# Kernel tuning notes

Measured on AMD Instinct MI355X. Metric: run time of the kernel, lower is better.

The kernel has to match this reference:

```python
import jax, jax.numpy as jnp
import numpy as np

N = 50000        # nodes
E = 500000       # undirected edges (stored once)
D = 64           # n_in_features
DOUT = 64        # n_out_features
HLF = 2          # hl_factor
NCONV = 3        # n_conv_its
H = D * HLF      # hidden width of conv MLPs


def setup_inputs() -> dict:
    key = jax.random.key(0)
    ks = jax.random.split(key, 8)
    s = 0.05
    edge_features = jax.random.normal(ks[0], (E, D), jnp.float32)
    edge_index = jax.random.randint(ks[1], (2, E), 0, N, dtype=jnp.int64)
    node_w1 = jax.random.normal(ks[2], (NCONV, 2 * D, H), jnp.float32) * s
    node_b1 = jnp.zeros((NCONV, H), jnp.float32)
    node_w2 = jax.random.normal(ks[3], (NCONV, H, D), jnp.float32) * s
    node_b2 = jnp.zeros((NCONV, D), jnp.float32)
    edge_w1 = jax.random.normal(ks[4], (2 * D, H), jnp.float32) * s
    edge_b1 = jnp.zeros((H,), jnp.float32)
    edge_w2 = jax.random.normal(ks[5], (H, DOUT), jnp.float32) * s
    edge_b2 = jnp.zeros((DOUT,), jnp.float32)
    return dict(edge_features=edge_features, edge_index=edge_index,
                node_w1=node_w1, node_b1=node_b1, node_w2=node_w2, node_b2=node_b2,
                edge_w1=edge_w1, edge_b1=edge_b1, edge_w2=edge_w2, edge_b2=edge_b2)


def _seg_mean(x, idx, n):
    s = jax.ops.segment_sum(x, idx, num_segments=n)
    c = jax.ops.segment_sum(jnp.ones((idx.shape[0], 1), x.dtype), idx, num_segments=n)
    return s / jnp.maximum(c, 1.0)


def reference(edge_features, edge_index, node_w1, node_b1, node_w2, node_b2,
              edge_w1, edge_b1, edge_w2, edge_b2):
    src, dst = edge_index[0], edge_index[1]
    # bidirectional (symmetrized) edges for message passing
    bi_src = jnp.concatenate([src, dst])
    bi_dst = jnp.concatenate([dst, src])

    # EdgeConvNoNodes: node feature = mean of incident edge features
    x = _seg_mean(jnp.concatenate([edge_features, edge_features], axis=0), bi_dst, N)  # [N, D]

    # NodeConv layers with residual: message = MLP(cat[x_i, x_j]), mean-aggregated
    for i in range(NCONV):
        m = jnp.concatenate([x[bi_dst], x[bi_src]], axis=-1)        # [2E, 2D]
        m = jax.nn.relu(m @ node_w1[i] + node_b1[i])                # [2E, H]
        m = jax.nn.relu(m @ node_w2[i] + node_b2[i])                # [2E, D]
        x = x + _seg_mean(m, bi_dst, N)

    # EdgeConv: symmetric edge MLP over node endpoint pairs + symmetry side loss
    def emlp(a, b):
        h = jax.nn.relu(jnp.concatenate([a, b], axis=-1) @ edge_w1 + edge_b1)
        return h @ edge_w2 + edge_b2

    e1 = emlp(x[src], x[dst])   # [E, DOUT]
    e2 = emlp(x[dst], x[src])   # [E, DOUT]
    edge_out = 0.5 * (e1 + e2)
    side_loss = jnp.mean((e1 - e2) ** 2)
    return edge_out, side_loss
```

## Files before the change

kernel.cpp:

```cpp
#include <hip/hip_runtime.h>


#define NN 50000
#define NE 500000
#define DE 1000000
#define NEB 7813

typedef __attribute__((ext_vector_type(8))) __bf16 bfrag;
typedef __attribute__((ext_vector_type(8))) short  svec8;
typedef __attribute__((ext_vector_type(4))) float  f32x4;

__device__ __forceinline__ unsigned short f2bf(float f){
  unsigned u = __builtin_bit_cast(unsigned, f);
  u += 0x7fffu + ((u >> 16) & 1u);
  return (unsigned short)(u >> 16);
}
__device__ __forceinline__ float bf2f(unsigned short s){
  return __builtin_bit_cast(float, ((unsigned)s) << 16);
}
#define MFMA __builtin_amdgcn_mfma_f32_16x16x32_bf16

__device__ __forceinline__ bfrag hbuild(const unsigned short* __restrict__ p,
                                        const unsigned short* __restrict__ q){
  svec8 pv = *(const svec8*)p;
  svec8 qv = *(const svec8*)q;
  bfrag r;
  #pragma unroll
  for (int i = 0; i < 8; i++){
    float f = bf2f((unsigned short)pv[i]) + bf2f((unsigned short)qv[i]);
    f = f > 0.f ? f : 0.f;
    r[i] = (__bf16)f;
  }
  return r;
}

__global__ void k_hist(const int* __restrict__ ei, int* __restrict__ cnt){
  int e = blockIdx.x*256 + threadIdx.x;
  if (e >= DE) return;
  int dst = (e < NE) ? ei[NE + e] : ei[e - NE];
  atomicAdd(&cnt[dst], 1);
}

__global__ void k_scan(const int* __restrict__ cnt, int* __restrict__ off,
                       int* __restrict__ cur, float* __restrict__ dinv){
  __shared__ int wsum[16];
  const int CH = 49;
  int tid = threadIdx.x;
  int base = tid * CH;
  int s = 0;
  for (int i = 0; i < CH; i++){
    int idx = base + i;
    if (idx < NN) s += cnt[idx];
  }
  int lane = tid & 63, w = tid >> 6;
  int inc = s;
  for (int o2 = 1; o2 < 64; o2 <<= 1){
    int t = __shfl_up(inc, o2);
    if (lane >= o2) inc += t;
  }
  if (lane == 63) wsum[w] = inc;
  __syncthreads();
  if (tid < 16){
    int v = wsum[tid], p = v;
    for (int o2 = 1; o2 < 16; o2 <<= 1){
      int t = __shfl_up(p, o2, 16);
      if (tid >= o2) p += t;
    }
    wsum[tid] = p - v;
  }
  __syncthreads();
  int pre = wsum[w] + inc - s;
  for (int i = 0; i < CH; i++){
    int idx = base + i;
    if (idx < NN){
      int v = cnt[idx];
      off[idx] = pre; cur[idx] = pre;
      dinv[idx] = 1.0f / (float)(v > 1 ? v : 1);
      pre += v;
    }
  }
  if (tid == 0) off[NN] = DE;
}

__global__ void k_fill(const int* __restrict__ ei, int* __restrict__ cur,
                       int* __restrict__ nbr, int* __restrict__ dstA, int* __restrict__ eid){
  int e = blockIdx.x*256 + threadIdx.x;
  if (e >= DE) return;
  int s, d, id;
  if (e < NE){ s = ei[e];  d = ei[NE + e]; id = e;      }
  else       { s = ei[e];  d = ei[e - NE]; id = e - NE; }
  int pos = atomicAdd(&cur[d], 1);
  nbr[pos] = s; dstA[pos] = d; eid[pos] = id;
}

__global__ void k_pack(const float* __restrict__ nw1, const float* __restrict__ nw2,
                       const float* __restrict__ ew1, const float* __restrict__ ew2,
                       unsigned short* __restrict__ wp){
  int t = blockIdx.x*256 + threadIdx.x;
  if (t >= 98304) return;
  const float* src; int NO, p, base;
  if (t < 49152)      { int l = t/16384;            src = nw1 + l*16384; NO=128; p = t - l*16384;      base = t - p; }
  else if (t < 73728) { int q = t-49152; int l=q/8192; src = nw2 + l*8192; NO=64; p = q - l*8192;      base = t - p; }
  else if (t < 90112) {                              src = ew1;           NO=128; p = t - 73728;       base = 73728; }
  else                {                              src = ew2;           NO=64;  p = t - 90112;       base = 90112; }
  int f = p >> 9, r = p & 511, lane = r >> 3, i = r & 7;
  int NB = NO >> 4, kb = f / NB, nb = f - kb*NB;
  int k = kb*32 + ((lane >> 4) << 3) + i;
  int c = nb*16 + (lane & 15);
  wp[base + p] = f2bf(src[k*NO + c]);
}

__global__ void k_init(const float* __restrict__ ef, const int* __restrict__ off,
                       const int* __restrict__ eid, const float* __restrict__ dinv,
                       float* __restrict__ x, unsigned short* __restrict__ xbf){
  int n = blockIdx.x*4 + (threadIdx.x >> 6);
  int lane = threadIdx.x & 63;
  if (n >= NN) return;
  int s0 = off[n], s1 = off[n+1];
  float acc = 0.f;
  for (int s = s0; s < s1; s++) acc += ef[eid[s]*64 + lane];
  float v = acc * dinv[n];
  x[n*64 + lane] = v;
  xbf[n*64 + lane] = f2bf(v);
}

__global__ __launch_bounds__(256,2) void k_pq(
    const unsigned short* __restrict__ xbf,
    const unsigned short* __restrict__ wp, int w1off,
    const float* __restrict__ bias,
    unsigned short* __restrict__ pb, unsigned short* __restrict__ qb)
{
  int lane = threadIdx.x & 63, wid = threadIdx.x >> 6;
  int tile = (blockIdx.x*4 + wid) * 32;
  if (tile >= NN) return;
  int r16 = lane & 15, g = lane >> 4;
  const svec8* w1g = (const svec8*)(wp + w1off);
  bfrag a[2][2];
  #pragma unroll
  for (int rb = 0; rb < 2; rb++){
    int n = tile + rb*16 + r16; if (n >= NN) n = NN-1;
    #pragma unroll
    for (int kb = 0; kb < 2; kb++)
      a[rb][kb] = __builtin_bit_cast(bfrag, *(const svec8*)(xbf + n*64 + kb*32 + g*8));
  }
  for (int ph = 0; ph < 2; ph++){
    f32x4 acc[8][2];
    #pragma unroll
    for (int nb = 0; nb < 8; nb++){ acc[nb][0] = (f32x4){0,0,0,0}; acc[nb][1] = (f32x4){0,0,0,0}; }
    #pragma unroll
    for (int kb = 0; kb < 2; kb++){
      #pragma unroll
      for (int nb = 0; nb < 8; nb++){
        bfrag b = __builtin_bit_cast(bfrag, w1g[((ph*2+kb)*8+nb)*64 + lane]);
        acc[nb][0] = MFMA(a[0][kb], b, acc[nb][0], 0, 0, 0);
        acc[nb][1] = MFMA(a[1][kb], b, acc[nb][1], 0, 0, 0);
      }
    }
    unsigned short* ob = ph ? qb : pb;
    #pragma unroll
    for (int nb = 0; nb < 8; nb++){
      float bv = (ph == 0) ? bias[nb*16 + r16] : 0.f;
      #pragma unroll
      for (int rb = 0; rb < 2; rb++){
        #pragma unroll
        for (int j = 0; j < 4; j++){
          int n = tile + rb*16 + g*4 + j;
          if (n < NN) ob[n*128 + nb*16 + r16] = f2bf(acc[nb][rb][j] + bv);
        }
      }
    }
  }
}

__global__ __launch_bounds__(256,4) void k_conv(
    const unsigned short* __restrict__ pb, const unsigned short* __restrict__ qb,
    const int* __restrict__ cdst, const int* __restrict__ cnbr,
    const unsigned short* __restrict__ wp, int w2off,
    const float* __restrict__ b2, float* __restrict__ xsum)
{
  int lane = threadIdx.x & 63, wid = threadIdx.x >> 6;
  int tile = (blockIdx.x*4 + wid) * 32;
  if (tile >= DE) return;
  int r16 = lane & 15, g = lane >> 4;
  int dr = cdst[tile + (lane & 31)];
  int d0 = cdst[tile + r16],      d1 = cdst[tile + 16 + r16];
  int s0 = cnbr[tile + r16],      s1 = cnbr[tile + 16 + r16];
  const svec8* w2g = (const svec8*)(wp + w2off);

  f32x4 acc[4][2];
  #pragma unroll
  for (int nb = 0; nb < 4; nb++){ acc[nb][0] = (f32x4){0,0,0,0}; acc[nb][1] = (f32x4){0,0,0,0}; }

  #pragma unroll
  for (int kb = 0; kb < 4; kb++){
    int off = kb*32 + g*8;
    bfrag h0 = hbuild(pb + d0*128 + off, qb + s0*128 + off);
    bfrag h1 = hbuild(pb + d1*128 + off, qb + s1*128 + off);
    #pragma unroll
    for (int nb = 0; nb < 4; nb++){
      bfrag b = __builtin_bit_cast(bfrag, w2g[(kb*4+nb)*64 + lane]);
      acc[nb][0] = MFMA(h0, b, acc[nb][0], 0, 0, 0);
      acc[nb][1] = MFMA(h1, b, acc[nb][1], 0, 0, 0);
    }
  }
  float m[4][2][4];
  #pragma unroll
  for (int nb = 0; nb < 4; nb++){
    float bv = b2[nb*16 + r16];
    #pragma unroll
    for (int rb = 0; rb < 2; rb++){
      #pragma unroll
      for (int j = 0; j < 4; j++){
        float v = acc[nb][rb][j] + bv;
        m[nb][rb][j] = v > 0.f ? v : 0.f;
      }
    }
  }
  int prev = __shfl_up(dr, 1);
  bool flag = (lane < 32) && (lane == 0 || dr != prev);
  unsigned long long mask = __ballot(flag);
  while (mask){
    int s = (int)__builtin_ctzll(mask);
    mask &= mask - 1;
    int e = mask ? (int)__builtin_ctzll(mask) : 32;
    int dseg = __shfl(dr, s);
    float p0 = 0.f, p1 = 0.f, p2 = 0.f, p3 = 0.f;
    #pragma unroll
    for (int rb = 0; rb < 2; rb++){
      #pragma unroll
      for (int j = 0; j < 4; j++){
        int row = rb*16 + g*4 + j;
        if ((unsigned)(row - s) < (unsigned)(e - s)){
          p0 += m[0][rb][j]; p1 += m[1][rb][j]; p2 += m[2][rb][j]; p3 += m[3][rb][j];
        }
      }
    }
    p0 += __shfl_xor(p0, 16); p0 += __shfl_xor(p0, 32);
    p1 += __shfl_xor(p1, 16); p1 += __shfl_xor(p1, 32);
    p2 += __shfl_xor(p2, 16); p2 += __shfl_xor(p2, 32);
    p3 += __shfl_xor(p3, 16); p3 += __shfl_xor(p3, 32);
    if (g == 0){
      atomicAdd(&xsum[dseg*64 +      r16], p0);
      atomicAdd(&xsum[dseg*64 + 16 + r16], p1);
      atomicAdd(&xsum[dseg*64 + 32 + r16], p2);
      atomicAdd(&xsum[dseg*64 + 48 + r16], p3);
    }
  }
}

__global__ void k_finish(const float* __restrict__ xsum, const float* __restrict__ dinv,
                         float* __restrict__ x, unsigned short* __restrict__ xbf){
  int n = blockIdx.x*4 + (threadIdx.x >> 6);
  int lane = threadIdx.x & 63;
  if (n >= NN) return;
  float v = x[n*64 + lane] + xsum[n*64 + lane] * dinv[n];
  x[n*64 + lane] = v;
  xbf[n*64 + lane] = f2bf(v);
}

__global__ __launch_bounds__(256,4) void k_edge(
    const unsigned short* __restrict__ pe, const unsigned short* __restrict__ qe,
    const int* __restrict__ ei,
    const unsigned short* __restrict__ wp,
    const float* __restrict__ b2,
    float* __restrict__ outp, float* __restrict__ part)
{
  __shared__ float wred[4];
  int lane = threadIdx.x & 63, wid = threadIdx.x >> 6;
  int tile = (blockIdx.x*4 + wid) * 16;
  bool valid = tile < NE;
  int tl = valid ? tile : 0;
  int r16 = lane & 15, g = lane >> 4;
  const svec8* w2g = (const svec8*)(wp + 90112);
  int el = tl + r16;
  int sn = ei[el], dn = ei[NE + el];

  f32x4 acc[4][2];
  #pragma unroll
  for (int nb = 0; nb < 4; nb++){ acc[nb][0] = (f32x4){0,0,0,0}; acc[nb][1] = (f32x4){0,0,0,0}; }

  #pragma unroll
  for (int kb = 0; kb < 4; kb++){
    int off = kb*32 + g*8;
    bfrag h0 = hbuild(pe + sn*128 + off, qe + dn*128 + off);
    bfrag h1 = hbuild(pe + dn*128 + off, qe + sn*128 + off);
    #pragma unroll
    for (int nb = 0; nb < 4; nb++){
      bfrag b = __builtin_bit_cast(bfrag, w2g[(kb*4+nb)*64 + lane]);
      acc[nb][0] = MFMA(h0, b, acc[nb][0], 0, 0, 0);
      acc[nb][1] = MFMA(h1, b, acc[nb][1], 0, 0, 0);
    }
  }
  float lsum = 0.f;
  #pragma unroll
  for (int nb = 0; nb < 4; nb++){
    float bv = b2[nb*16 + r16];
    #pragma unroll
    for (int j = 0; j < 4; j++){
      float v1 = acc[nb][0][j] + bv;
      float v2 = acc[nb][1][j] + bv;
      int e = tile + g*4 + j;
      if (valid) outp[e*64 + nb*16 + r16] = 0.5f*(v1 + v2);
      float d = v1 - v2; lsum += d*d;
    }
  }
  if (!valid) lsum = 0.f;
  for (int o2 = 32; o2 > 0; o2 >>= 1) lsum += __shfl_down(lsum, o2);
  if (lane == 0) wred[wid] = lsum;
  __syncthreads();
  if (threadIdx.x == 0) part[blockIdx.x] = wred[0] + wred[1] + wred[2] + wred[3];
}

__global__ void k_final(const float* __restrict__ part, float* __restrict__ outp){
  __shared__ float wred[16];
  int tid = threadIdx.x;
  float s = 0.f;
  for (int i = tid; i < NEB; i += 1024) s += part[i];
  for (int o2 = 32; o2 > 0; o2 >>= 1) s += __shfl_down(s, o2);
  int lane = tid & 63, w = tid >> 6;
  if (lane == 0) wred[w] = s;
  __syncthreads();
  if (tid == 0){
    float t = 0.f;
    #pragma unroll
    for (int i = 0; i < 16; i++) t += wred[i];
    outp[32000000] = t * (1.0f / 32000000.0f);
  }
}

extern "C" void kernel_launch(void* const* d_in, const int* in_sizes, int n_in,
                              void* d_out, int out_size, void* d_ws, size_t ws_size,
                              hipStream_t stream)
{
  const float* ef  = (const float*)d_in[0];
  const int*   ei  = (const int*)  d_in[1];
  const float* nw1 = (const float*)d_in[2];
  const float* nb1 = (const float*)d_in[3];
  const float* nw2 = (const float*)d_in[4];
  const float* nb2 = (const float*)d_in[5];
  const float* ew1 = (const float*)d_in[6];
  const float* eb1 = (const float*)d_in[7];
  const float* ew2 = (const float*)d_in[8];
  const float* eb2 = (const float*)d_in[9];
  float* outp = (float*)d_out;

  char* ws = (char*)d_ws;
  size_t o = 0;
  auto alloc = [&](size_t b)->char*{ char* p = ws + o; o += (b + 255) & ~(size_t)255; return p; };
  int*   cnt  = (int*)  alloc((size_t)NN*4);
  int*   off  = (int*)  alloc((size_t)(NN+1)*4);
  int*   cur  = (int*)  alloc((size_t)NN*4);
  float* dinv = (float*)alloc((size_t)NN*4);
  int*   nbr  = (int*)  alloc((size_t)DE*4);
  int*   dstA = (int*)  alloc((size_t)DE*4);
  int*   eid  = (int*)  alloc((size_t)DE*4);
  float* x    = (float*)alloc((size_t)NN*64*4);
  unsigned short* xbf = (unsigned short*)alloc((size_t)NN*64*2);
  unsigned short* wp  = (unsigned short*)alloc((size_t)98304*2);
  float* part = (float*)alloc((size_t)NEB*4);
  unsigned short* pbuf = (unsigned short*)alloc((size_t)NN*128*2);
  unsigned short* qbuf = (unsigned short*)alloc((size_t)NN*128*2);
  float* xs0  = (float*)alloc((size_t)NN*64*4);
  float* xs1  = (float*)alloc((size_t)NN*64*4);
  float* xs2  = (float*)alloc((size_t)NN*64*4);
  float* xsum[3] = {xs0, xs1, xs2};

  hipMemsetAsync(cnt, 0, (size_t)NN*4, stream);
  hipMemsetAsync(xs0, 0, (size_t)NN*64*4, stream);
  hipMemsetAsync(xs1, 0, (size_t)NN*64*4, stream);
  hipMemsetAsync(xs2, 0, (size_t)NN*64*4, stream);
  k_hist<<<(DE+255)/256, 256, 0, stream>>>(ei, cnt);
  k_scan<<<1, 1024, 0, stream>>>(cnt, off, cur, dinv);
  k_fill<<<(DE+255)/256, 256, 0, stream>>>(ei, cur, nbr, dstA, eid);
  k_pack<<<384, 256, 0, stream>>>(nw1, nw2, ew1, ew2, wp);
  k_init<<<NN/4, 256, 0, stream>>>(ef, off, eid, dinv, x, xbf);
  for (int l = 0; l < 3; l++){
    k_pq<<<391, 256, 0, stream>>>(xbf, wp, l*16384, nb1 + l*128, pbuf, qbuf);
    k_conv<<<DE/128 + 1, 256, 0, stream>>>(pbuf, qbuf, dstA, nbr, wp,
                                           49152 + l*8192, nb2 + l*64, xsum[l]);
    k_finish<<<NN/4 + 1, 256, 0, stream>>>(xsum[l], dinv, x, xbf);
  }
  k_pq<<<391, 256, 0, stream>>>(xbf, wp, 73728, eb1, pbuf, qbuf);
  k_edge<<<NEB, 256, 0, stream>>>(pbuf, qbuf, ei, wp, eb2, outp, part);
  k_final<<<1, 1024, 0, stream>>>(part, outp);
}
```

Measured before the change: 827.1 us.

## Parallelize initial edge-mean via segmented atomic reduction and coalesce scan loop

```diff
diff --git a/kernel.cpp b/kernel.cpp
--- a/kernel.cpp
+++ b/kernel.cpp
@@ -44,40 +44,37 @@
 __global__ void k_scan(const int* __restrict__ cnt, int* __restrict__ off,
                        int* __restrict__ cur, float* __restrict__ dinv){
   __shared__ int wsum[16];
-  const int CH = 49;
+  __shared__ int carry_s;
   int tid = threadIdx.x;
-  int base = tid * CH;
-  int s = 0;
-  for (int i = 0; i < CH; i++){
-    int idx = base + i;
-    if (idx < NN) s += cnt[idx];
-  }
   int lane = tid & 63, w = tid >> 6;
-  int inc = s;
-  for (int o2 = 1; o2 < 64; o2 <<= 1){
-    int t = __shfl_up(inc, o2);
-    if (lane >= o2) inc += t;
-  }
-  if (lane == 63) wsum[w] = inc;
-  __syncthreads();
-  if (tid < 16){
-    int v = wsum[tid], p = v;
-    for (int o2 = 1; o2 < 16; o2 <<= 1){
-      int t = __shfl_up(p, o2, 16);
-      if (tid >= o2) p += t;
-    }
-    wsum[tid] = p - v;
-  }
-  __syncthreads();
-  int pre = wsum[w] + inc - s;
-  for (int i = 0; i < CH; i++){
-    int idx = base + i;
+  int carry = 0;
+  for (int base = 0; base < NN; base += 1024){
+    int idx = base + tid;
+    int v = (idx < NN) ? cnt[idx] : 0;
+    int inc = v;
+    for (int o2 = 1; o2 < 64; o2 <<= 1){
+      int t = __shfl_up(inc, o2);
+      if (lane >= o2) inc += t;
+    }
+    if (lane == 63) wsum[w] = inc;
+    __syncthreads();
+    if (tid < 16){
+      int vv = wsum[tid], p = vv;
+      for (int o2 = 1; o2 < 16; o2 <<= 1){
+        int t = __shfl_up(p, o2, 16);
+        if (tid >= o2) p += t;
+      }
+      wsum[tid] = p - vv;
+    }
+    __syncthreads();
+    int ex = carry + wsum[w] + inc - v;
     if (idx < NN){
-      int v = cnt[idx];
-      off[idx] = pre; cur[idx] = pre;
+      off[idx] = ex; cur[idx] = ex;
       dinv[idx] = 1.0f / (float)(v > 1 ? v : 1);
-      pre += v;
-    }
+    }
+    if (tid == 1023) carry_s = carry + wsum[15] + inc;
+    __syncthreads();
+    carry = carry_s;
   }
   if (tid == 0) off[NN] = DE;
 }
@@ -110,16 +107,57 @@
   wp[base + p] = f2bf(src[k*NO + c]);
 }
 
-__global__ void k_init(const float* __restrict__ ef, const int* __restrict__ off,
-                       const int* __restrict__ eid, const float* __restrict__ dinv,
-                       float* __restrict__ x, unsigned short* __restrict__ xbf){
+__global__ __launch_bounds__(256,4) void k_init(
+    const float* __restrict__ ef, const int* __restrict__ dstA,
+    const int* __restrict__ eid, float* __restrict__ xsum)
+{
+  int lane = threadIdx.x & 63, wid = threadIdx.x >> 6;
+  int tile = (blockIdx.x*4 + wid) * 32;
+  if (tile >= DE) return;
+  int q = lane >> 4, c4 = lane & 15;
+  int dr = dstA[tile + (lane & 31)];
+  int er = eid[tile + (lane & 31)];
+  f32x4 v[8];
+  #pragma unroll
+  for (int it = 0; it < 8; it++){
+    int row = q + it*4;
+    int e = __shfl(er, row);
+    v[it] = *(const f32x4*)(ef + (size_t)e*64 + c4*4);
+  }
+  int prev = __shfl_up(dr, 1);
+  bool flag = (lane < 32) && (lane == 0 || dr != prev);
+  unsigned long long mask = __ballot(flag);
+  while (mask){
+    int s = (int)__builtin_ctzll(mask);
+    mask &= mask - 1;
+    int e = mask ? (int)__builtin_ctzll(mask) : 32;
+    int dseg = __shfl(dr, s);
+    f32x4 p = {0,0,0,0};
+    #pragma unroll
+    for (int it = 0; it < 8; it++){
+      int row = q + it*4;
+      if ((unsigned)(row - s) < (unsigned)(e - s)) p += v[it];
+    }
+    #pragma unroll
+    for (int k = 0; k < 4; k++){
+      p[k] += __shfl_xor(p[k], 16);
+      p[k] += __shfl_xor(p[k], 32);
+    }
+    if (q == 0){
+      atomicAdd(&xsum[dseg*64 + c4*4 + 0], p[0]);
+      atomicAdd(&xsum[dseg*64 + c4*4 + 1], p[1]);
+      atomicAdd(&xsum[dseg*64 + c4*4 + 2], p[2]);
+      atomicAdd(&xsum[dseg*64 + c4*4 + 3], p[3]);
+    }
+  }
+}
+
+__global__ void k_div(const float* __restrict__ xsum, const float* __restrict__ dinv,
+                      float* __restrict__ x, unsigned short* __restrict__ xbf){
   int n = blockIdx.x*4 + (threadIdx.x >> 6);
   int lane = threadIdx.x & 63;
   if (n >= NN) return;
-  int s0 = off[n], s1 = off[n+1];
-  float acc = 0.f;
-  for (int s = s0; s < s1; s++) acc += ef[eid[s]*64 + lane];
-  float v = acc * dinv[n];
+  float v = xsum[n*64 + lane] * dinv[n];
   x[n*64 + lane] = v;
   xbf[n*64 + lane] = f2bf(v);
 }
@@ -360,12 +398,14 @@
   float* part = (float*)alloc((size_t)NEB*4);
   unsigned short* pbuf = (unsigned short*)alloc((size_t)NN*128*2);
   unsigned short* qbuf = (unsigned short*)alloc((size_t)NN*128*2);
+  float* xsI  = (float*)alloc((size_t)NN*64*4);
   float* xs0  = (float*)alloc((size_t)NN*64*4);
   float* xs1  = (float*)alloc((size_t)NN*64*4);
   float* xs2  = (float*)alloc((size_t)NN*64*4);
   float* xsum[3] = {xs0, xs1, xs2};
 
   hipMemsetAsync(cnt, 0, (size_t)NN*4, stream);
+  hipMemsetAsync(xsI, 0, (size_t)NN*64*4, stream);
   hipMemsetAsync(xs0, 0, (size_t)NN*64*4, stream);
   hipMemsetAsync(xs1, 0, (size_t)NN*64*4, stream);
   hipMemsetAsync(xs2, 0, (size_t)NN*64*4, stream);
@@ -373,7 +413,8 @@
   k_scan<<<1, 1024, 0, stream>>>(cnt, off, cur, dinv);
   k_fill<<<(DE+255)/256, 256, 0, stream>>>(ei, cur, nbr, dstA, eid);
   k_pack<<<384, 256, 0, stream>>>(nw1, nw2, ew1, ew2, wp);
-  k_init<<<NN/4, 256, 0, stream>>>(ef, off, eid, dinv, x, xbf);
+  k_init<<<NEB, 256, 0, stream>>>(ef, dstA, eid, xsI);
+  k_div<<<NN/4 + 1, 256, 0, stream>>>(xsI, dinv, x, xbf);
   for (int l = 0; l < 3; l++){
     k_pq<<<391, 256, 0, stream>>>(xbf, wp, l*16384, nb1 + l*128, pbuf, qbuf);
     k_conv<<<DE/128 + 1, 256, 0, stream>>>(pbuf, qbuf, dstA, nbr, wp,
```

Result: faster. 700.1 us (-15.4%).
